# Performance work log

Hardware: AMD Instinct MI355X
Metric: run time of the kernel (lower is better)

## Reference

```python
import jax, jax.numpy as jnp
import numpy as np

HIDDEN = 128
HEADS = 8
HEAD_DIM = HIDDEN // HEADS
N = 2048
SCALE = HEAD_DIM ** -0.5


def setup_inputs() -> dict:
    key = jax.random.key(0)
    ks = jax.random.split(key, 12)
    # xavier_uniform bound for square (HIDDEN, HIDDEN) weights
    bound = float(np.sqrt(6.0 / (HIDDEN + HIDDEN)))
    def w(k):
        return jax.random.uniform(k, (HIDDEN, HIDDEN), jnp.float32, -bound, bound)
    return {
        "x": jax.random.normal(ks[0], (N, HIDDEN), jnp.float32),
        "attention_bias": jax.random.normal(ks[1], (N, N, HEADS), jnp.float32),
        "key_padding_mask": jnp.zeros((N,), jnp.bool_),
        "Wq": w(ks[2]), "bq": jnp.zeros((HIDDEN,), jnp.float32),
        "Wk": w(ks[3]), "bk": jnp.zeros((HIDDEN,), jnp.float32),
        "Wv": w(ks[4]), "bv": jnp.zeros((HIDDEN,), jnp.float32),
        "Wo": w(ks[5]), "bo": jnp.zeros((HIDDEN,), jnp.float32),
    }


def reference(x, attention_bias, key_padding_mask, Wq, bq, Wk, bk, Wv, bv, Wo, bo):
    n = x.shape[0]
    # torch Linear: y = x @ W.T + b
    q = (x @ Wq.T + bq).reshape(n, HEADS, HEAD_DIM).transpose(1, 0, 2)  # (H, N, D)
    k = (x @ Wk.T + bk).reshape(n, HEADS, HEAD_DIM).transpose(1, 0, 2)
    v = (x @ Wv.T + bv).reshape(n, HEADS, HEAD_DIM).transpose(1, 0, 2)
    scores = jnp.einsum('hnd,hmd->hnm', q, k) * SCALE        # (H, N, N)
    scores = scores + attention_bias.transpose(2, 0, 1)       # additive graph bias
    mask = key_padding_mask[None, None, :]                    # (1, 1, N) over keys
    scores = jnp.where(mask, -jnp.inf, scores)
    attn = jax.nn.softmax(scores, axis=-1)
    out = jnp.einsum('hnm,hmd->hnd', attn, v)                 # (H, N, D)
    out = out.transpose(1, 0, 2).reshape(n, HIDDEN)
    return out @ Wo.T + bo
```

## Files before the change

### kernel.cpp

```cpp
#include <hip/hip_runtime.h>
#include <hip/hip_bf16.h>

#define NSEQ 2048
#define HID 128
#define HEADS 8
#define HD 16
#define SCALE 0.25f
#define TQ 16
#define TK 64
#define SPLIT 8
#define KT_PER (NSEQ / TK / SPLIT)
#define QROW 160
#define PM_W 36
#define PH_W (16 * PM_W + 4)

typedef unsigned short ushort_t;
typedef __attribute__((ext_vector_type(8))) short short8;
typedef __attribute__((ext_vector_type(4))) float floatx4;

__device__ __forceinline__ void unpack2(unsigned u, float& a, float& b) {
    union { unsigned x; float f; } lo, hi;
    lo.x = u << 16; hi.x = u & 0xffff0000u;
    a = lo.f; b = hi.f;
}
__device__ __forceinline__ void unpack8(uint4 u, float* f) {
    unpack2(u.x, f[0], f[1]); unpack2(u.y, f[2], f[3]);
    unpack2(u.z, f[4], f[5]); unpack2(u.w, f[6], f[7]);
}
__device__ __forceinline__ unsigned pack_bf16x2(float a, float b) {
    __hip_bfloat16 ba = __float2bfloat16(a);
    __hip_bfloat16 bb = __float2bfloat16(b);
    return (unsigned)*(ushort_t*)&ba | ((unsigned)*(ushort_t*)&bb << 16);
}

__global__ void transpose_kernel(const float* __restrict__ Wq, const float* __restrict__ Wk,
                                 const float* __restrict__ Wv, const float* __restrict__ Wo,
                                 float* __restrict__ wt)
{
    int idx = blockIdx.x * 256 + threadIdx.x;
    int w = idx >> 14, rem = idx & 16383;
    int row = rem >> 7, col = rem & 127;
    const float* W = (w == 0) ? Wq : (w == 1) ? Wk : (w == 2) ? Wv : Wo;
    wt[w * 16384 + col * HID + row] = W[rem];
}

__global__ __launch_bounds__(128) void qkv_kernel(
    const float* __restrict__ x, const float* __restrict__ WqT,
    const float* __restrict__ WkT, const float* __restrict__ WvT,
    const float* __restrict__ bq, const float* __restrict__ bk,
    const float* __restrict__ bv, float* __restrict__ Qm,
    __hip_bfloat16* __restrict__ Kb, __hip_bfloat16* __restrict__ Vt)
{
    __shared__ float xs[8 * HID];
    const int j = threadIdx.x;
    const int mat = blockIdx.x >> 8;
    const int rb = blockIdx.x & 255;
    const int r0 = rb * 8;
    const float* WT = (mat == 0) ? WqT : (mat == 1) ? WkT : WvT;
    const float* bb = (mat == 0) ? bq : (mat == 1) ? bk : bv;
    const float4* xg = (const float4*)(x + (size_t)r0 * HID);
    float4* xl = (float4*)xs;
    for (int i = j; i < 8 * HID / 4; i += 128) xl[i] = xg[i];
    __syncthreads();
    float acc[8];
#pragma unroll
    for (int r = 0; r < 8; ++r) acc[r] = 0.f;
#pragma unroll 4
    for (int i = 0; i < HID; ++i) {
        float w = WT[i * HID + j];
#pragma unroll
        for (int r = 0; r < 8; ++r) acc[r] = fmaf(xs[r * HID + i], w, acc[r]);
    }
    float bv_ = bb[j];
#pragma unroll
    for (int r = 0; r < 8; ++r) acc[r] += bv_;
    if (mat == 0) {
#pragma unroll
        for (int r = 0; r < 8; ++r) Qm[(size_t)(r0 + r) * HID + j] = acc[r];
    } else if (mat == 1) {
#pragma unroll
        for (int r = 0; r < 8; ++r) Kb[(size_t)(r0 + r) * HID + j] = __float2bfloat16(acc[r]);
    } else {
        unsigned u[4];
#pragma unroll
        for (int p = 0; p < 4; ++p) u[p] = pack_bf16x2(acc[2 * p], acc[2 * p + 1]);
        *(uint4*)((ushort_t*)Vt + (size_t)j * NSEQ + r0) = make_uint4(u[0], u[1], u[2], u[3]);
    }
}

__global__ __launch_bounds__(256, 4) void attn_kernel(
    const float* __restrict__ Qm, const __hip_bfloat16* __restrict__ Kb,
    const __hip_bfloat16* __restrict__ Vt, const float* __restrict__ bias,
    const unsigned char* __restrict__ mask, float* __restrict__ Op,
    float* __restrict__ Lp)
{
    __shared__ float qs[TQ * QROW];
    __shared__ float Pbuf[8 * PH_W];
    __shared__ float wl[4 * TQ * HEADS];

    const int t = threadIdx.x;
    const int lane = t & 63;
    const int wid = t >> 6;
    const int qb = blockIdx.x & 127;
    const int sp = blockIdx.x >> 7;
    const int n0 = qb * TQ;

    const int sc_mp = t >> 3;
    const int sc_h  = t & 7;
    const int kk = wid & 1;
    const int hbase = (wid >> 1) * 4;
    const int frag_m = lane & 15;
    const int frag_q = lane >> 4;

    {
        for (int idx = t; idx < 512; idx += 256) {
            int r = idx >> 5, c = idx & 31;
            int h = c >> 2, dg = c & 3;
            float4 v = ((const float4*)(Qm + (size_t)n0 * HID))[idx];
            *(float4*)&qs[r * QROW + h * 20 + dg * 4] = v;
        }
    }
    floatx4 acc[4];
#pragma unroll
    for (int hh = 0; hh < 4; ++hh) acc[hh] = (floatx4){0.f, 0.f, 0.f, 0.f};
    float lsum[TQ];
#pragma unroll
    for (int r = 0; r < TQ; ++r) lsum[r] = 0.0f;
    __syncthreads();

    for (int kt = 0; kt < KT_PER; ++kt) {
        const int m0 = (sp * KT_PER + kt) * TK;
        {
            const int m1 = m0 + sc_mp * 2;
            const ushort_t* kp = (const ushort_t*)Kb + (size_t)m1 * HID + sc_h * HD;
            uint4 ka = *(const uint4*)kp;
            uint4 kb2 = *(const uint4*)(kp + 8);
            uint4 kc = *(const uint4*)(kp + HID);
            uint4 kd = *(const uint4*)(kp + HID + 8);
            float k0[16], k1[16];
            unpack8(ka, k0); unpack8(kb2, k0 + 8);
            unpack8(kc, k1); unpack8(kd, k1 + 8);
            const bool msk0 = mask[m1] != 0;
            const bool msk1 = mask[m1 + 1] != 0;
            unsigned* Pw = (unsigned*)Pbuf;
#pragma unroll
            for (int rg = 0; rg < 2; ++rg) {
                float bb0[8], bb1[8];
                const float* bp = bias + (((size_t)(n0 + rg * 8)) * NSEQ + m1) * HEADS + sc_h;
#pragma unroll
                for (int rr = 0; rr < 8; ++rr) {
                    bb0[rr] = __builtin_nontemporal_load(bp + (size_t)rr * (NSEQ * HEADS));
                    bb1[rr] = __builtin_nontemporal_load(bp + (size_t)rr * (NSEQ * HEADS) + HEADS);
                }
#pragma unroll
                for (int rr = 0; rr < 8; ++rr) {
                    const int r = rg * 8 + rr;
                    const float* qr = &qs[r * QROW + sc_h * 20];
                    float qf[16];
                    *(float4*)&qf[0]  = *(const float4*)(qr);
                    *(float4*)&qf[4]  = *(const float4*)(qr + 4);
                    *(float4*)&qf[8]  = *(const float4*)(qr + 8);
                    *(float4*)&qf[12] = *(const float4*)(qr + 12);
                    float d0 = 0.f, d1 = 0.f;
#pragma unroll
                    for (int i = 0; i < 16; ++i) {
                        d0 = fmaf(qf[i], k0[i], d0);
                        d1 = fmaf(qf[i], k1[i], d1);
                    }
                    float s0 = fmaf(d0, SCALE, bb0[rr]);
                    float s1 = fmaf(d1, SCALE, bb1[rr]);
                    if (msk0) s0 = -INFINITY;
                    if (msk1) s1 = -INFINITY;
                    float e0 = __expf(s0);
                    float e1 = __expf(s1);
                    lsum[r] += e0 + e1;
                    Pw[sc_h * PH_W + r * PM_W + sc_mp] = pack_bf16x2(e0, e1);
                }
            }
        }
        __syncthreads();
        {
            const unsigned* Pw = (const unsigned*)Pbuf;
#pragma unroll
            for (int hh = 0; hh < 4; ++hh) {
                const int h = hbase + hh;
                const ushort_t* vrow = (const ushort_t*)Vt +
                    ((size_t)(h * HD + frag_m)) * NSEQ + m0 + kk * 32 + frag_q * 8;
                short8 bfrag = *(const short8*)vrow;
                short8 afrag = *(const short8*)&Pw[h * PH_W + frag_m * PM_W + kk * 16 + frag_q * 4];
                acc[hh] = __builtin_amdgcn_mfma_f32_16x16x32_bf16(afrag, bfrag, acc[hh], 0, 0, 0);
            }
        }
        __syncthreads();
    }

#pragma unroll
    for (int r = 0; r < TQ; ++r) {
        lsum[r] += __shfl_xor(lsum[r], 8);
        lsum[r] += __shfl_xor(lsum[r], 16);
        lsum[r] += __shfl_xor(lsum[r], 32);
    }
    if (lane < 8) {
#pragma unroll
        for (int r = 0; r < TQ; ++r)
            wl[wid * (TQ * HEADS) + r * 8 + lane] = lsum[r];
    }
    {
        float* obuf = Pbuf;
#pragma unroll
        for (int hh = 0; hh < 4; ++hh) {
#pragma unroll
            for (int reg = 0; reg < 4; ++reg) {
                int m = frag_q * 4 + reg;
                obuf[kk * 2048 + (hbase + hh) * 256 + m * 16 + frag_m] = acc[hh][reg];
            }
        }
    }
    __syncthreads();
    if (t < 128) {
        const float* obuf = Pbuf;
#pragma unroll
        for (int r = 0; r < TQ; ++r) {
            int h = t >> 4, d = t & 15;
            float v = obuf[h * 256 + r * 16 + d] + obuf[2048 + h * 256 + r * 16 + d];
            Op[((size_t)sp * NSEQ + n0 + r) * HID + t] = v;
        }
        const int r2 = t >> 3, h2 = t & 7;
        float l = wl[r2 * 8 + h2] + wl[128 + r2 * 8 + h2] +
                  wl[256 + r2 * 8 + h2] + wl[384 + r2 * 8 + h2];
        Lp[((size_t)sp * NSEQ + n0 + r2) * HEADS + h2] = l;
    }
}

__global__ __launch_bounds__(128) void proj_kernel(
    const float* __restrict__ Op, const float* __restrict__ Lp,
    const float* __restrict__ WoT, const float* __restrict__ bo,
    float* __restrict__ out)
{
    __shared__ float xs[4 * HID];
    const int j = threadIdx.x;
    const int r0 = blockIdx.x * 4;
    const int hh = j >> 4;
#pragma unroll
    for (int r = 0; r < 4; ++r) {
        const size_t n = r0 + r;
        float s = 0.f, l = 0.f;
#pragma unroll
        for (int sp = 0; sp < SPLIT; ++sp) {
            s += Op[((size_t)sp * NSEQ + n) * HID + j];
            l += Lp[((size_t)sp * NSEQ + n) * HEADS + hh];
        }
        xs[r * HID + j] = s / l;
    }
    __syncthreads();
    float acc[4];
#pragma unroll
    for (int r = 0; r < 4; ++r) acc[r] = 0.f;
#pragma unroll 4
    for (int i = 0; i < HID; ++i) {
        float w = WoT[i * HID + j];
#pragma unroll
        for (int r = 0; r < 4; ++r) acc[r] = fmaf(xs[r * HID + i], w, acc[r]);
    }
    float b = bo[j];
#pragma unroll
    for (int r = 0; r < 4; ++r)
        out[(size_t)(r0 + r) * HID + j] = acc[r] + b;
}

extern "C" void kernel_launch(void* const* d_in, const int* in_sizes, int n_in,
                              void* d_out, int out_size, void* d_ws, size_t ws_size,
                              hipStream_t stream) {
    const float* x    = (const float*)d_in[0];
    const float* bias = (const float*)d_in[1];
    const unsigned char* mask = (const unsigned char*)d_in[2];
    const float* Wq = (const float*)d_in[3];
    const float* bq = (const float*)d_in[4];
    const float* Wk = (const float*)d_in[5];
    const float* bk = (const float*)d_in[6];
    const float* Wv = (const float*)d_in[7];
    const float* bv = (const float*)d_in[8];
    const float* Wo = (const float*)d_in[9];
    const float* bo = (const float*)d_in[10];
    float* out = (float*)d_out;

    float* w = (float*)d_ws;
    float* WqT = w;
    float* WkT = w + 16384;
    float* WvT = w + 32768;
    float* WoT = w + 49152;
    float* Qm  = w + 65536;
    __hip_bfloat16* Kb = (__hip_bfloat16*)(w + 327680);
    __hip_bfloat16* Vt = (__hip_bfloat16*)(w + 458752);
    float* Op  = w + 589824;
    float* Lp  = w + 589824 + (size_t)SPLIT * NSEQ * HID;

    transpose_kernel<<<256, 256, 0, stream>>>(Wq, Wk, Wv, Wo, w);
    qkv_kernel<<<768, 128, 0, stream>>>(x, WqT, WkT, WvT, bq, bk, bv, Qm, Kb, Vt);
    attn_kernel<<<128 * SPLIT, 256, 0, stream>>>(Qm, Kb, Vt, bias, mask, Op, Lp);
    proj_kernel<<<512, 128, 0, stream>>>(Op, Lp, WoT, bo, out);
}
```

Before: 242.8 us.

## Compute QK scores with MFMA using split bf16 Q, register-resident softmax

The attention kernel now computes QK^T with 16x16x16 bf16 MFMA instead of scalar FMAs. Q is pre-scaled and split into high and low bf16 parts to keep accuracy, and the bias is fed in as the accumulator. Probabilities stay in registers and go straight into the PV MFMA, which removes the shared-memory P buffer and the block barriers. The key split rises from 8 to 16, doubling the partial outputs that the projection kernel must reduce. Bias loads become strided 4-byte reads per lane and are no longer nontemporal, which may hurt memory coalescing.

```diff
diff --git a/kernel.cpp b/kernel.cpp
--- a/kernel.cpp
+++ b/kernel.cpp
@@ -7,26 +7,14 @@
 #define HD 16
 #define SCALE 0.25f
 #define TQ 16
-#define TK 64
-#define SPLIT 8
-#define KT_PER (NSEQ / TK / SPLIT)
-#define QROW 160
-#define PM_W 36
-#define PH_W (16 * PM_W + 4)
+#define SPLIT 16
+#define KEYS_PER (NSEQ / SPLIT)
+#define KT16 (KEYS_PER / 16)
 
 typedef unsigned short ushort_t;
-typedef __attribute__((ext_vector_type(8))) short short8;
+typedef __attribute__((ext_vector_type(4))) short short4v;
 typedef __attribute__((ext_vector_type(4))) float floatx4;
 
-__device__ __forceinline__ void unpack2(unsigned u, float& a, float& b) {
-    union { unsigned x; float f; } lo, hi;
-    lo.x = u << 16; hi.x = u & 0xffff0000u;
-    a = lo.f; b = hi.f;
-}
-__device__ __forceinline__ void unpack8(uint4 u, float* f) {
-    unpack2(u.x, f[0], f[1]); unpack2(u.y, f[2], f[3]);
-    unpack2(u.z, f[4], f[5]); unpack2(u.w, f[6], f[7]);
-}
 __device__ __forceinline__ unsigned pack_bf16x2(float a, float b) {
     __hip_bfloat16 ba = __float2bfloat16(a);
     __hip_bfloat16 bb = __float2bfloat16(b);
@@ -48,7 +36,8 @@
     const float* __restrict__ x, const float* __restrict__ WqT,
     const float* __restrict__ WkT, const float* __restrict__ WvT,
     const float* __restrict__ bq, const float* __restrict__ bk,
-    const float* __restrict__ bv, float* __restrict__ Qm,
+    const float* __restrict__ bv,
+    __hip_bfloat16* __restrict__ Qh, __hip_bfloat16* __restrict__ Ql,
     __hip_bfloat16* __restrict__ Kb, __hip_bfloat16* __restrict__ Vt)
 {
     __shared__ float xs[8 * HID];
@@ -76,7 +65,14 @@
     for (int r = 0; r < 8; ++r) acc[r] += bv_;
     if (mat == 0) {
 #pragma unroll
-        for (int r = 0; r < 8; ++r) Qm[(size_t)(r0 + r) * HID + j] = acc[r];
+        for (int r = 0; r < 8; ++r) {
+            float qsv = acc[r] * SCALE;
+            __hip_bfloat16 hb = __float2bfloat16(qsv);
+            float hf = __bfloat162float(hb);
+            __hip_bfloat16 lb = __float2bfloat16(qsv - hf);
+            Qh[(size_t)(r0 + r) * HID + j] = hb;
+            Ql[(size_t)(r0 + r) * HID + j] = lb;
+        }
     } else if (mat == 1) {
 #pragma unroll
         for (int r = 0; r < 8; ++r) Kb[(size_t)(r0 + r) * HID + j] = __float2bfloat16(acc[r]);
@@ -89,146 +85,78 @@
 }
 
 __global__ __launch_bounds__(256, 4) void attn_kernel(
-    const float* __restrict__ Qm, const __hip_bfloat16* __restrict__ Kb,
-    const __hip_bfloat16* __restrict__ Vt, const float* __restrict__ bias,
-    const unsigned char* __restrict__ mask, float* __restrict__ Op,
-    float* __restrict__ Lp)
-{
-    __shared__ float qs[TQ * QROW];
-    __shared__ float Pbuf[8 * PH_W];
-    __shared__ float wl[4 * TQ * HEADS];
-
+    const __hip_bfloat16* __restrict__ Qh, const __hip_bfloat16* __restrict__ Ql,
+    const __hip_bfloat16* __restrict__ Kb, const __hip_bfloat16* __restrict__ Vt,
+    const float* __restrict__ bias, const unsigned char* __restrict__ mask,
+    float* __restrict__ Op, float* __restrict__ Lp)
+{
     const int t = threadIdx.x;
     const int lane = t & 63;
     const int wid = t >> 6;
+    const int qi = lane & 15;
+    const int g = lane >> 4;
     const int qb = blockIdx.x & 127;
     const int sp = blockIdx.x >> 7;
     const int n0 = qb * TQ;
-
-    const int sc_mp = t >> 3;
-    const int sc_h  = t & 7;
-    const int kk = wid & 1;
-    const int hbase = (wid >> 1) * 4;
-    const int frag_m = lane & 15;
-    const int frag_q = lane >> 4;
-
-    {
-        for (int idx = t; idx < 512; idx += 256) {
-            int r = idx >> 5, c = idx & 31;
-            int h = c >> 2, dg = c & 3;
-            float4 v = ((const float4*)(Qm + (size_t)n0 * HID))[idx];
-            *(float4*)&qs[r * QROW + h * 20 + dg * 4] = v;
+    const int m0 = sp * KEYS_PER;
+    const int h0 = wid * 2;
+
+    short4v qhf[2], qlf[2];
+#pragma unroll
+    for (int hh = 0; hh < 2; ++hh) {
+        const size_t qoff = (size_t)(n0 + qi) * HID + (h0 + hh) * HD + 4 * g;
+        qhf[hh] = *(const short4v*)((const ushort_t*)Qh + qoff);
+        qlf[hh] = *(const short4v*)((const ushort_t*)Ql + qoff);
+    }
+
+    floatx4 o[2];
+    o[0] = (floatx4){0.f, 0.f, 0.f, 0.f};
+    o[1] = (floatx4){0.f, 0.f, 0.f, 0.f};
+    float lrun[2] = {0.f, 0.f};
+
+    const float* bias_base = bias + (size_t)(n0 + qi) * NSEQ * HEADS;
+
+#pragma unroll 2
+    for (int kt = 0; kt < KT16; ++kt) {
+        const int m1 = m0 + kt * 16;
+        const uchar4 mk = *(const uchar4*)(mask + m1 + 4 * g);
+#pragma unroll
+        for (int hh = 0; hh < 2; ++hh) {
+            const int h = h0 + hh;
+            short4v ka = *(const short4v*)((const ushort_t*)Kb +
+                         (size_t)(m1 + qi) * HID + h * HD + 4 * g);
+            const float* bp = bias_base + (size_t)(m1 + 4 * g) * HEADS + h;
+            floatx4 s;
+            s.x = bp[0]; s.y = bp[8]; s.z = bp[16]; s.w = bp[24];
+            s = __builtin_amdgcn_mfma_f32_16x16x16bf16_1k(ka, qhf[hh], s, 0, 0, 0);
+            s = __builtin_amdgcn_mfma_f32_16x16x16bf16_1k(ka, qlf[hh], s, 0, 0, 0);
+            float e0 = mk.x ? 0.f : __expf(s.x);
+            float e1 = mk.y ? 0.f : __expf(s.y);
+            float e2 = mk.z ? 0.f : __expf(s.z);
+            float e3 = mk.w ? 0.f : __expf(s.w);
+            lrun[hh] += (e0 + e1) + (e2 + e3);
+            __hip_bfloat16 p0 = __float2bfloat16(e0);
+            __hip_bfloat16 p1 = __float2bfloat16(e1);
+            __hip_bfloat16 p2 = __float2bfloat16(e2);
+            __hip_bfloat16 p3 = __float2bfloat16(e3);
+            short4v pa = {(short)*(ushort_t*)&p0, (short)*(ushort_t*)&p1,
+                          (short)*(ushort_t*)&p2, (short)*(ushort_t*)&p3};
+            short4v vb = *(const short4v*)((const ushort_t*)Vt +
+                         (size_t)(h * HD + qi) * NSEQ + m1 + 4 * g);
+            o[hh] = __builtin_amdgcn_mfma_f32_16x16x16bf16_1k(pa, vb, o[hh], 0, 0, 0);
         }
     }
-    floatx4 acc[4];
-#pragma unroll
-    for (int hh = 0; hh < 4; ++hh) acc[hh] = (floatx4){0.f, 0.f, 0.f, 0.f};
-    float lsum[TQ];
-#pragma unroll
-    for (int r = 0; r < TQ; ++r) lsum[r] = 0.0f;
-    __syncthreads();
-
-    for (int kt = 0; kt < KT_PER; ++kt) {
-        const int m0 = (sp * KT_PER + kt) * TK;
-        {
-            const int m1 = m0 + sc_mp * 2;
-            const ushort_t* kp = (const ushort_t*)Kb + (size_t)m1 * HID + sc_h * HD;
-            uint4 ka = *(const uint4*)kp;
-            uint4 kb2 = *(const uint4*)(kp + 8);
-            uint4 kc = *(const uint4*)(kp + HID);
-            uint4 kd = *(const uint4*)(kp + HID + 8);
-            float k0[16], k1[16];
-            unpack8(ka, k0); unpack8(kb2, k0 + 8);
-            unpack8(kc, k1); unpack8(kd, k1 + 8);
-            const bool msk0 = mask[m1] != 0;
-            const bool msk1 = mask[m1 + 1] != 0;
-            unsigned* Pw = (unsigned*)Pbuf;
-#pragma unroll
-            for (int rg = 0; rg < 2; ++rg) {
-                float bb0[8], bb1[8];
-                const float* bp = bias + (((size_t)(n0 + rg * 8)) * NSEQ + m1) * HEADS + sc_h;
-#pragma unroll
-                for (int rr = 0; rr < 8; ++rr) {
-                    bb0[rr] = __builtin_nontemporal_load(bp + (size_t)rr * (NSEQ * HEADS));
-                    bb1[rr] = __builtin_nontemporal_load(bp + (size_t)rr * (NSEQ * HEADS) + HEADS);
-                }
-#pragma unroll
-                for (int rr = 0; rr < 8; ++rr) {
-                    const int r = rg * 8 + rr;
-                    const float* qr = &qs[r * QROW + sc_h * 20];
-                    float qf[16];
-                    *(float4*)&qf[0]  = *(const float4*)(qr);
-                    *(float4*)&qf[4]  = *(const float4*)(qr + 4);
-                    *(float4*)&qf[8]  = *(const float4*)(qr + 8);
-                    *(float4*)&qf[12] = *(const float4*)(qr + 12);
-                    float d0 = 0.f, d1 = 0.f;
-#pragma unroll
-                    for (int i = 0; i < 16; ++i) {
-                        d0 = fmaf(qf[i], k0[i], d0);
-                        d1 = fmaf(qf[i], k1[i], d1);
-                    }
-                    float s0 = fmaf(d0, SCALE, bb0[rr]);
-                    float s1 = fmaf(d1, SCALE, bb1[rr]);
-                    if (msk0) s0 = -INFINITY;
-                    if (msk1) s1 = -INFINITY;
-                    float e0 = __expf(s0);
-                    float e1 = __expf(s1);
-                    lsum[r] += e0 + e1;
-                    Pw[sc_h * PH_W + r * PM_W + sc_mp] = pack_bf16x2(e0, e1);
-                }
-            }
-        }
-        __syncthreads();
-        {
-            const unsigned* Pw = (const unsigned*)Pbuf;
-#pragma unroll
-            for (int hh = 0; hh < 4; ++hh) {
-                const int h = hbase + hh;
-                const ushort_t* vrow = (const ushort_t*)Vt +
-                    ((size_t)(h * HD + frag_m)) * NSEQ + m0 + kk * 32 + frag_q * 8;
-                short8 bfrag = *(const short8*)vrow;
-                short8 afrag = *(const short8*)&Pw[h * PH_W + frag_m * PM_W + kk * 16 + frag_q * 4];
-                acc[hh] = __builtin_amdgcn_mfma_f32_16x16x32_bf16(afrag, bfrag, acc[hh], 0, 0, 0);
-            }
-        }
-        __syncthreads();
-    }
-
-#pragma unroll
-    for (int r = 0; r < TQ; ++r) {
-        lsum[r] += __shfl_xor(lsum[r], 8);
-        lsum[r] += __shfl_xor(lsum[r], 16);
-        lsum[r] += __shfl_xor(lsum[r], 32);
-    }
-    if (lane < 8) {
-#pragma unroll
-        for (int r = 0; r < TQ; ++r)
-            wl[wid * (TQ * HEADS) + r * 8 + lane] = lsum[r];
-    }
-    {
-        float* obuf = Pbuf;
-#pragma unroll
-        for (int hh = 0; hh < 4; ++hh) {
-#pragma unroll
-            for (int reg = 0; reg < 4; ++reg) {
-                int m = frag_q * 4 + reg;
-                obuf[kk * 2048 + (hbase + hh) * 256 + m * 16 + frag_m] = acc[hh][reg];
-            }
-        }
-    }
-    __syncthreads();
-    if (t < 128) {
-        const float* obuf = Pbuf;
-#pragma unroll
-        for (int r = 0; r < TQ; ++r) {
-            int h = t >> 4, d = t & 15;
-            float v = obuf[h * 256 + r * 16 + d] + obuf[2048 + h * 256 + r * 16 + d];
-            Op[((size_t)sp * NSEQ + n0 + r) * HID + t] = v;
-        }
-        const int r2 = t >> 3, h2 = t & 7;
-        float l = wl[r2 * 8 + h2] + wl[128 + r2 * 8 + h2] +
-                  wl[256 + r2 * 8 + h2] + wl[384 + r2 * 8 + h2];
-        Lp[((size_t)sp * NSEQ + n0 + r2) * HEADS + h2] = l;
+
+#pragma unroll
+    for (int hh = 0; hh < 2; ++hh) {
+        lrun[hh] += __shfl_xor(lrun[hh], 16);
+        lrun[hh] += __shfl_xor(lrun[hh], 32);
+        const int h = h0 + hh;
+#pragma unroll
+        for (int r = 0; r < 4; ++r)
+            Op[((size_t)sp * NSEQ + n0 + 4 * g + r) * HID + h * HD + qi] = o[hh][r];
+        if (g == 0)
+            Lp[((size_t)sp * NSEQ + n0 + qi) * HEADS + h] = lrun[hh];
     }
 }
 
@@ -289,14 +217,15 @@
     float* WkT = w + 16384;
     float* WvT = w + 32768;
     float* WoT = w + 49152;
-    float* Qm  = w + 65536;
+    __hip_bfloat16* Qh = (__hip_bfloat16*)(w + 65536);
+    __hip_bfloat16* Ql = (__hip_bfloat16*)(w + 196608);
     __hip_bfloat16* Kb = (__hip_bfloat16*)(w + 327680);
     __hip_bfloat16* Vt = (__hip_bfloat16*)(w + 458752);
     float* Op  = w + 589824;
     float* Lp  = w + 589824 + (size_t)SPLIT * NSEQ * HID;
 
     transpose_kernel<<<256, 256, 0, stream>>>(Wq, Wk, Wv, Wo, w);
-    qkv_kernel<<<768, 128, 0, stream>>>(x, WqT, WkT, WvT, bq, bk, bv, Qm, Kb, Vt);
-    attn_kernel<<<128 * SPLIT, 256, 0, stream>>>(Qm, Kb, Vt, bias, mask, Op, Lp);
+    qkv_kernel<<<768, 128, 0, stream>>>(x, WqT, WkT, WvT, bq, bk, bv, Qh, Ql, Kb, Vt);
+    attn_kernel<<<128 * SPLIT, 256, 0, stream>>>(Qh, Ql, Kb, Vt, bias, mask, Op, Lp);
     proj_kernel<<<512, 128, 0, stream>>>(Op, Lp, WoT, bo, out);
 }
```

After: 296.6 us. +22.2%, slower.
